# Kernel tuning notes

Hardware: AMD Instinct MI355X
Metric: run time of the kernel (lower is better)

The kernel has to match this reference:

```python
import jax, jax.numpy as jnp
import numpy as np

# Module hyperparameters (init_kwargs)
RADIUS = 0.3
NSAMPLE = 64
NORMALIZE_XYZ = True

B, N, M, C = 8, 20000, 1024, 128  # batch, points, centers, feature channels


def setup_inputs() -> dict:
    key = jax.random.key(0)
    k1, k2, k3, k4, k5 = jax.random.split(key, 5)
    # points uniform in a side-2 cube -> each radius-0.3 ball holds ~280 pts
    xyz = jax.random.uniform(k1, (B, N, 3), jnp.float32) * 2.0
    new_xyz = jax.random.uniform(k2, (B, M, 3), jnp.float32) * 2.0
    batch_distances = jax.random.uniform(k3, (B, M), jnp.float32)
    inds = jax.random.randint(k4, (B, M), 0, N, jnp.int64)
    features = jax.random.normal(k5, (B, C, N), jnp.float32)
    return {"xyz": xyz, "new_xyz": new_xyz, "batch_distances": batch_distances,
            "inds": inds, "features": features}


def ball_query(xyz, new_xyz):
    """Standard pointnet2 ball query: first NSAMPLE indices with d^2 < r^2,
    remaining slots filled with the first in-range index. -> (B, M, NSAMPLE) int32."""
    n = xyz.shape[1]
    # (B, M, N) squared distances
    d2 = jnp.sum((new_xyz[:, :, None, :] - xyz[:, None, :, :]) ** 2, axis=-1)
    mask = d2 < (RADIUS * RADIUS)
    ar = jnp.arange(n, dtype=jnp.int32)
    # sort key: valid indices keep their index (in order), invalid pushed to back
    sort_key = jnp.where(mask, ar, ar + n)
    order = jnp.argsort(sort_key, axis=-1)[..., :NSAMPLE].astype(jnp.int32)
    cnt = jnp.sum(mask, axis=-1)  # (B, M) number of in-range points
    slot = jnp.arange(NSAMPLE, dtype=cnt.dtype)
    # slots beyond cnt are filled with the first valid index (0 if cnt == 0)
    idx = jnp.where(slot[None, None, :] < jnp.maximum(cnt, 1)[..., None],
                    order, order[..., :1])
    return idx


def reference(xyz, new_xyz, batch_distances, inds, features):
    # batch_distances / inds only accelerate the original cpp kernel; the math
    # is the plain radius search below.
    idx = ball_query(xyz, new_xyz)  # (B, M, S)
    # group xyz: (B, M, S, 3) -> (B, 3, M, S)
    grouped_xyz = jax.vmap(lambda pts, i: pts[i])(xyz, idx)
    grouped_xyz = jnp.transpose(grouped_xyz, (0, 3, 1, 2))
    grouped_xyz = grouped_xyz - jnp.transpose(new_xyz, (0, 2, 1))[..., None]
    if NORMALIZE_XYZ:
        grouped_xyz = grouped_xyz / RADIUS
    # group features: (B, C, M, S)
    grouped_features = jax.vmap(lambda f, i: f[:, i])(features, idx)
    new_features = jnp.concatenate([grouped_xyz, grouped_features], axis=1)
    return (new_features, idx)
```

## Files before the change

### kernel.cpp

```cpp
#include <hip/hip_runtime.h>

#define B_ 8
#define N_ 20000
#define M_ 1024
#define C_ 128
#define S_ 64
#define NCH_ 131
#define TILE_ 512

typedef float  vf4 __attribute__((ext_vector_type(4)));

__global__ __launch_bounds__(256) void query_kernel(
    const float* __restrict__ xyz,
    const float* __restrict__ new_xyz,
    float* __restrict__ out,
    int* __restrict__ iws)
{
    const int wid  = threadIdx.x >> 6;
    const int lane = threadIdx.x & 63;
    const int bm   = blockIdx.x * 4 + wid;
    const int b    = bm >> 10;
    const int m    = bm & (M_ - 1);

    __shared__ int s_idx[4][S_];

    const float cx = new_xyz[bm * 3 + 0];
    const float cy = new_xyz[bm * 3 + 1];
    const float cz = new_xyz[bm * 3 + 2];
    const float r2 = (float)(0.3 * 0.3);
    const float* xb = xyz + (size_t)b * N_ * 3;
    const unsigned long long below = (1ull << lane) - 1ull;

#define LOAD_TILE(F, INB, NB, BASE) do {                                      \
    NB = (BASE) + 8 * lane;                                                   \
    INB = (NB < N_);        \
    if (INB) {                                                                \
        const float4* p4_ = (const float4*)(xb + (size_t)NB * 3);             \
        _Pragma("unroll")                                                     \
        for (int q = 0; q < 6; ++q) {                                         \
            const float4 v_ = p4_[q];                                         \
            F[4*q+0] = v_.x; F[4*q+1] = v_.y; F[4*q+2] = v_.z; F[4*q+3] = v_.w; \
        }                                                                     \
    } } while (0)

#define PROC_TILE(F, INB, NB) do {                                            \
    unsigned vbits = 0;                                                       \
    if (INB) {                                                                \
        _Pragma("unroll")                                                     \
        for (int j = 0; j < 8; ++j) {                                         \
            const float dx = __fadd_rn(F[3*j+0], -cx);                        \
            const float dy = __fadd_rn(F[3*j+1], -cy);                        \
            const float dz = __fadd_rn(F[3*j+2], -cz);                        \
            const float d2 = __fadd_rn(                                       \
                __fadd_rn(__fmul_rn(dx, dx), __fmul_rn(dy, dy)),              \
                __fmul_rn(dz, dz));                                           \
            if (d2 < r2) vbits |= (1u << j);                                  \
        }                                                                     \
    }                                                                         \
    int pre = 0, tot = 0;                                                     \
    _Pragma("unroll")                                                         \
    for (int j = 0; j < 8; ++j) {                                             \
        const unsigned long long mk = __ballot((vbits >> j) & 1u);            \
        pre += __popcll(mk & below);                                          \
        tot += __popcll(mk);                                                  \
    }                                                                         \
    int pos = cnt + pre;                                                      \
    _Pragma("unroll")                                                         \
    for (int j = 0; j < 8; ++j) {                                             \
        if (vbits & (1u << j)) {                                              \
            if (pos < S_) s_idx[wid][pos] = NB + j;                           \
            ++pos;                                                            \
        }                                                                     \
    }                                                                         \
    cnt += tot; } while (0)

    int cnt = 0;
    float fA[24], fB[24];
    bool inbA = false, inbB = false;
    int nA = 0, nB = 0;

    LOAD_TILE(fA, inbA, nA, 0);
    int base = 0;
    for (;;) {
        {
            const int nxt = base + TILE_;
            const bool have = (nxt < N_);
            if (have) LOAD_TILE(fB, inbB, nB, nxt);
            PROC_TILE(fA, inbA, nA);
            base = nxt;
            if (cnt >= S_ || !have) break;
        }
        {
            const int nxt = base + TILE_;
            const bool have = (nxt < N_);
            if (have) LOAD_TILE(fA, inbA, nA, nxt);
            PROC_TILE(fB, inbB, nB);
            base = nxt;
            if (cnt >= S_ || !have) break;
        }
    }
#undef LOAD_TILE
#undef PROC_TILE

    const int c = cnt < S_ ? cnt : S_;
    const int first = (c > 0) ? s_idx[wid][0] : 0;
    if (lane >= c) s_idx[wid][lane] = first;

    const int n = s_idx[wid][lane];

    float* out_idx = out + (size_t)B_ * NCH_ * M_ * S_;
    __builtin_nontemporal_store((float)n, &out_idx[(size_t)bm * S_ + lane]);
    iws[(size_t)bm * S_ + lane] = n;

    const float px = xb[n * 3 + 0];
    const float py = xb[n * 3 + 1];
    const float pz = xb[n * 3 + 2];
    __builtin_nontemporal_store((px - cx) / 0.3f,
        &out[(((size_t)b * NCH_ + 0) * M_ + m) * S_ + lane]);
    __builtin_nontemporal_store((py - cy) / 0.3f,
        &out[(((size_t)b * NCH_ + 1) * M_ + m) * S_ + lane]);
    __builtin_nontemporal_store((pz - cz) / 0.3f,
        &out[(((size_t)b * NCH_ + 2) * M_ + m) * S_ + lane]);
}

__global__ __launch_bounds__(256) void group_feat_kernel(
    const float* __restrict__ features,
    const int* __restrict__ iws,
    float* __restrict__ out)
{
    const int b  = blockIdx.x & 7;
    const int ch = blockIdx.x >> 3;

    __shared__ float slice[N_];

    const float* fb = features + ((size_t)b * C_ + ch) * N_;
    const vf4* fb4 = (const vf4*)fb;
    vf4* sl4 = (vf4*)slice;
    for (int i = threadIdx.x; i < N_ / 4; i += 256)
        sl4[i] = __builtin_nontemporal_load(&fb4[i]);
    __syncthreads();

    const int* ib = iws + (size_t)b * M_ * S_;
    float* ob = out + ((size_t)b * NCH_ + 3 + ch) * (size_t)(M_ * S_);
    for (int e = threadIdx.x * 4; e < M_ * S_; e += 256 * 4) {
        const int4 ii = *(const int4*)(ib + e);
        vf4 w;
        w.x = slice[ii.x]; w.y = slice[ii.y];
        w.z = slice[ii.z]; w.w = slice[ii.w];
        __builtin_nontemporal_store(w, (vf4*)(ob + e));
    }
}

__global__ __launch_bounds__(256) void qg_fused(
    const float* __restrict__ xyz,
    const float* __restrict__ new_xyz,
    const float* __restrict__ features,
    float* __restrict__ out)
{
    const int bm = blockIdx.x;
    const int b  = bm >> 10;
    const int m  = bm & (M_ - 1);
    const int tid = threadIdx.x;

    __shared__ int s_idx[S_];

    if (tid < 64) {
        const int lane = tid;
        const float cx = new_xyz[bm * 3 + 0];
        const float cy = new_xyz[bm * 3 + 1];
        const float cz = new_xyz[bm * 3 + 2];
        const float r2 = (float)(0.3 * 0.3);
        const float* xb = xyz + (size_t)b * N_ * 3;

        int cnt = 0;
        for (int base = 0; base < N_; base += 64) {
            const int n = base + lane;
            bool valid = false;
            if (n < N_) {
                const float dx = __fadd_rn(xb[n * 3 + 0], -cx);
                const float dy = __fadd_rn(xb[n * 3 + 1], -cy);
                const float dz = __fadd_rn(xb[n * 3 + 2], -cz);
                const float d2 = __fadd_rn(
                    __fadd_rn(__fmul_rn(dx, dx), __fmul_rn(dy, dy)),
                    __fmul_rn(dz, dz));
                valid = d2 < r2;
            }
            const unsigned long long mk = __ballot(valid);
            if (valid) {
                const int pos = cnt + __popcll(mk & ((1ull << lane) - 1ull));
                if (pos < S_) s_idx[pos] = n;
            }
            cnt += __popcll(mk);
            if (cnt >= S_) break;
        }
        const int c = cnt < S_ ? cnt : S_;
        const int first = (c > 0) ? s_idx[0] : 0;
        if (lane >= c) s_idx[lane] = first;

        float* out_idx = out + (size_t)B_ * NCH_ * M_ * S_;
        out_idx[(size_t)bm * S_ + lane] = (float)s_idx[lane];
    }
    __syncthreads();

    if (tid < 3 * S_) {
        const int ch = tid >> 6;
        const int s  = tid & 63;
        const int n  = s_idx[s];
        const float v = (xyz[((size_t)b * N_ + n) * 3 + ch] - new_xyz[bm * 3 + ch]) / 0.3f;
        out[(((size_t)b * NCH_ + ch) * M_ + m) * S_ + s] = v;
    }

    const int s  = tid & 63;
    const int cq = tid >> 6;
    const int n  = s_idx[s];
    const float* fb = features + (size_t)b * C_ * N_;
    float* ob = out + (((size_t)b * NCH_ + 3) * M_ + m) * S_ + s;
    for (int ch = cq; ch < C_; ch += 4) {
        ob[(size_t)ch * (M_ * S_)] = fb[(size_t)ch * N_ + n];
    }
}

extern "C" void kernel_launch(void* const* d_in, const int* in_sizes, int n_in,
                              void* d_out, int out_size, void* d_ws, size_t ws_size,
                              hipStream_t stream) {
    const float* xyz      = (const float*)d_in[0];
    const float* new_xyz  = (const float*)d_in[1];
    const float* features = (const float*)d_in[4];
    float* out = (float*)d_out;

    const size_t need = (size_t)B_ * M_ * S_ * sizeof(int);
    if (ws_size < need) {
        qg_fused<<<B_ * M_, 256, 0, stream>>>(xyz, new_xyz, features, out);
        return;
    }
    int* iws = (int*)d_ws;

    query_kernel<<<(B_ * M_) / 4, 256, 0, stream>>>(xyz, new_xyz, out, iws);
    group_feat_kernel<<<B_ * C_, 256, 0, stream>>>(features, iws, out);
}
```

Before: 135.0 us.

## Split ball query across four waves per center with block-level prefix merge

Assigns one 256-thread block per query center instead of one wave, with each wave scanning a 512-point slice of a 2048-point chunk. Per-wave hit counts are combined through shared memory and a block barrier to keep the ordered first-64 selection. This shortens the serial early-exit scan latency per center, at the cost of a __syncthreads per chunk and four times as many blocks. The final xyz grouping is spread across 192 threads.

After: 131.2 us. 1.03x faster.

```diff
diff --git a/kernel.cpp b/kernel.cpp
--- a/kernel.cpp
+++ b/kernel.cpp
@@ -6,7 +6,8 @@
 #define C_ 128
 #define S_ 64
 #define NCH_ 131
-#define TILE_ 512
+#define CHUNK_ 2048
+#define NCHK_ ((N_ + CHUNK_ - 1) / CHUNK_)
 
 typedef float  vf4 __attribute__((ext_vector_type(4)));
 
@@ -16,13 +17,15 @@
     float* __restrict__ out,
     int* __restrict__ iws)
 {
-    const int wid  = threadIdx.x >> 6;
-    const int lane = threadIdx.x & 63;
-    const int bm   = blockIdx.x * 4 + wid;
+    const int tid  = threadIdx.x;
+    const int wid  = tid >> 6;
+    const int lane = tid & 63;
+    const int bm   = blockIdx.x;
     const int b    = bm >> 10;
     const int m    = bm & (M_ - 1);
 
-    __shared__ int s_idx[4][S_];
+    __shared__ int s_idx[S_];
+    __shared__ int s_tot[2][4];
 
     const float cx = new_xyz[bm * 3 + 0];
     const float cy = new_xyz[bm * 3 + 1];
@@ -31,8 +34,8 @@
     const float* xb = xyz + (size_t)b * N_ * 3;
     const unsigned long long below = (1ull << lane) - 1ull;
 
-#define LOAD_TILE(F, INB, NB, BASE) do {                                      \
-    NB = (BASE) + 8 * lane;                                                   \
+#define LOAD_TILE(F, INB, NB, CB) do {                                        \
+    NB = (CB) + (wid << 9) + (lane << 3);                                     \
     INB = (NB < N_);        \
     if (INB) {                                                                \
         const float4* p4_ = (const float4*)(xb + (size_t)NB * 3);             \
@@ -43,7 +46,7 @@
         }                                                                     \
     } } while (0)
 
-#define PROC_TILE(F, INB, NB) do {                                            \
+#define PROC_TILE(F, INB, NB, PAR) do {                                       \
     unsigned vbits = 0;                                                       \
     if (INB) {                                                                \
         _Pragma("unroll")                                                     \
@@ -64,15 +67,29 @@
         pre += __popcll(mk & below);                                          \
         tot += __popcll(mk);                                                  \
     }                                                                         \
-    int pos = cnt + pre;                                                      \
+    if (lane == 0) s_tot[PAR][wid] = tot;                                     \
+    __syncthreads();                                                          \
+    int off = cnt;                                                            \
+    _Pragma("unroll")                                                         \
+    for (int w = 0; w < 4; ++w) { if (w < wid) off += s_tot[PAR][w]; }        \
+    int pos = off + pre;                                                      \
     _Pragma("unroll")                                                         \
     for (int j = 0; j < 8; ++j) {                                             \
         if (vbits & (1u << j)) {                                              \
-            if (pos < S_) s_idx[wid][pos] = NB + j;                           \
+            if (pos < S_) s_idx[pos] = NB + j;                                \
             ++pos;                                                            \
         }                                                                     \
     }                                                                         \
-    cnt += tot; } while (0)
+    cnt += s_tot[PAR][0] + s_tot[PAR][1] + s_tot[PAR][2] + s_tot[PAR][3];     \
+    } while (0)
+
+#define STAGE(PF, PINB, PNB, RF, RINB, RNB, PAR) do {                         \
+    if (t_load < NCHK_) { LOAD_TILE(RF, RINB, RNB, t_load * CHUNK_); }        \
+    ++t_load;                                                                 \
+    PROC_TILE(PF, PINB, PNB, PAR);                                            \
+    ++t_proc;                                                                 \
+    if (cnt >= S_ || t_proc >= NCHK_) goto qdone;                             \
+    } while (0)
 
     int cnt = 0;
     float fA[24], fB[24];
@@ -80,47 +97,40 @@
     int nA = 0, nB = 0;
 
     LOAD_TILE(fA, inbA, nA, 0);
-    int base = 0;
+    int t_load = 1, t_proc = 0;
+
     for (;;) {
-        {
-            const int nxt = base + TILE_;
-            const bool have = (nxt < N_);
-            if (have) LOAD_TILE(fB, inbB, nB, nxt);
-            PROC_TILE(fA, inbA, nA);
-            base = nxt;
-            if (cnt >= S_ || !have) break;
-        }
-        {
-            const int nxt = base + TILE_;
-            const bool have = (nxt < N_);
-            if (have) LOAD_TILE(fA, inbA, nA, nxt);
-            PROC_TILE(fB, inbB, nB);
-            base = nxt;
-            if (cnt >= S_ || !have) break;
-        }
-    }
+        STAGE(fA, inbA, nA, fB, inbB, nB, 0);
+        STAGE(fB, inbB, nB, fA, inbA, nA, 1);
+    }
+qdone:
 #undef LOAD_TILE
 #undef PROC_TILE
-
-    const int c = cnt < S_ ? cnt : S_;
-    const int first = (c > 0) ? s_idx[wid][0] : 0;
-    if (lane >= c) s_idx[wid][lane] = first;
-
-    const int n = s_idx[wid][lane];
-
-    float* out_idx = out + (size_t)B_ * NCH_ * M_ * S_;
-    __builtin_nontemporal_store((float)n, &out_idx[(size_t)bm * S_ + lane]);
-    iws[(size_t)bm * S_ + lane] = n;
-
-    const float px = xb[n * 3 + 0];
-    const float py = xb[n * 3 + 1];
-    const float pz = xb[n * 3 + 2];
-    __builtin_nontemporal_store((px - cx) / 0.3f,
-        &out[(((size_t)b * NCH_ + 0) * M_ + m) * S_ + lane]);
-    __builtin_nontemporal_store((py - cy) / 0.3f,
-        &out[(((size_t)b * NCH_ + 1) * M_ + m) * S_ + lane]);
-    __builtin_nontemporal_store((pz - cz) / 0.3f,
-        &out[(((size_t)b * NCH_ + 2) * M_ + m) * S_ + lane]);
+#undef STAGE
+
+    __syncthreads();
+    {
+        const int c = cnt < S_ ? cnt : S_;
+        const int first = (c > 0) ? s_idx[0] : 0;
+        if (tid >= c && tid < S_) s_idx[tid] = first;
+    }
+    __syncthreads();
+
+    if (tid < S_) {
+        const int n = s_idx[tid];
+        float* out_idx = out + (size_t)B_ * NCH_ * M_ * S_;
+        __builtin_nontemporal_store((float)n, &out_idx[(size_t)bm * S_ + tid]);
+        iws[(size_t)bm * S_ + tid] = n;
+    }
+    if (tid < 3 * S_) {
+        const int ch = tid >> 6;
+        const int s  = tid & 63;
+        const int n  = s_idx[s];
+        const float cc = new_xyz[bm * 3 + ch];
+        const float v = (xb[n * 3 + ch] - cc) / 0.3f;
+        __builtin_nontemporal_store(v,
+            &out[(((size_t)b * NCH_ + ch) * M_ + m) * S_ + s]);
+    }
 }
 
 __global__ __launch_bounds__(256) void group_feat_kernel(
@@ -235,6 +245,6 @@
     }
     int* iws = (int*)d_ws;
 
-    query_kernel<<<(B_ * M_) / 4, 256, 0, stream>>>(xyz, new_xyz, out, iws);
+    query_kernel<<<B_ * M_, 256, 0, stream>>>(xyz, new_xyz, out, iws);
     group_feat_kernel<<<B_ * C_, 256, 0, stream>>>(features, iws, out);
 }
```
